# Performance work log

Hardware: AMD Instinct MI355X
Metric: run time of the kernel (lower is better)

Reference implementation:

```python
import jax, jax.numpy as jnp
import numpy as np


def setup_inputs() -> dict:
    key0 = jax.random.key(0)
    kq, kk, kv = jax.random.split(key0, 3)
    B, H, L, S, D = 2, 8, 2048, 2048, 64
    query = jax.random.normal(kq, (B, H, L, D), dtype=jnp.float32)
    key = jax.random.normal(kk, (B, H, S, D), dtype=jnp.float32)
    value = jax.random.normal(kv, (B, H, S, D), dtype=jnp.float32)
    return {"query": query, "key": key, "value": value}


def reference(query, key, value):
    # Original computes matmul(q[b,h,l,1,d,1], k[b,h,1,s,1,d]) -> [B,H,L,S,D,D]
    # outer products, divides by sqrt(query.shape[-1]) AFTER unsqueeze (==1, no-op),
    # then sums dims (4,5). That is algebraically exactly rowsum(q)*rowsum(k).
    qsum = query.sum(axis=-1)                       # [B,H,L]
    ksum = key.sum(axis=-1)                         # [B,H,S]
    score = qsum[..., :, None] * ksum[..., None, :]  # [B,H,L,S]
    attn = jax.nn.softmax(score, axis=-1)            # softmax over S
    out = jnp.einsum('bhls,bhsd->bhld', attn, value)  # [B,H,L,D]
    return out
```

## Files before the change

kernel.cpp:

```cpp
#include <hip/hip_runtime.h>
#include <hip/hip_bf16.h>

#define BH 16
#define L 2048
#define S 2048
#define DD 64
#define BM 64
#define BK 64
#define LDSPAD 8
#define LDW (BK + LDSPAD)

typedef __attribute__((ext_vector_type(4))) float f32x4;
typedef __bf16 bf16x8 __attribute__((ext_vector_type(8)));

union FragU {
  bf16x8 f;
  __hip_bfloat162 h2[4];
};

__device__ inline __hip_bfloat162 exp2pack(float al2, float nsl2, float k0,
                                           float k1, float& d) {
  float e0 = __builtin_amdgcn_exp2f(fmaf(al2, k0, nsl2));
  float e1 = __builtin_amdgcn_exp2f(fmaf(al2, k1, nsl2));
  d += e0 + e1;
  return __float22bfloat162_rn(make_float2(e0, e1));
}

__global__ __launch_bounds__(256) void prep_kernel(
    const float* __restrict__ k, const float* __restrict__ v,
    float* __restrict__ ks, __hip_bfloat16* __restrict__ vt) {
  __shared__ __hip_bfloat16 tile[DD][LDW];
  int t = threadIdx.x;
  if (blockIdx.x < 2048) {
    int g = blockIdx.x * 256 + t;
    int row = g >> 4;
    int l16 = g & 15;
    float4 x = reinterpret_cast<const float4*>(k + (size_t)row * DD)[l16];
    float s = x.x + x.y + x.z + x.w;
    s += __shfl_xor(s, 1);
    s += __shfl_xor(s, 2);
    s += __shfl_xor(s, 4);
    s += __shfl_xor(s, 8);
    if (l16 == 0) ks[row] = s;
  } else {
    int bid = blockIdx.x - 2048;
    int s0 = (bid & 31) * 64;
    int bh = bid >> 5;
    int srow = t >> 4;
    int d4 = (t & 15) * 4;
#pragma unroll
    for (int kk = 0; kk < 4; ++kk) {
      int s = srow + kk * 16;
      float4 val = *reinterpret_cast<const float4*>(
          v + ((size_t)(bh * S + s0 + s)) * DD + d4);
      tile[d4 + 0][s] = __float2bfloat16(val.x);
      tile[d4 + 1][s] = __float2bfloat16(val.y);
      tile[d4 + 2][s] = __float2bfloat16(val.z);
      tile[d4 + 3][s] = __float2bfloat16(val.w);
    }
    __syncthreads();
    int dd = t >> 3;
    int j = t & 7;
#pragma unroll
    for (int kk = 0; kk < 2; ++kk) {
      int d = dd + kk * 32;
      uint4 val = *reinterpret_cast<const uint4*>(&tile[d][j * 8]);
      *reinterpret_cast<uint4*>(vt + ((size_t)(bh * DD + d)) * S + s0 + j * 8) =
          val;
    }
  }
}

__global__ __launch_bounds__(256) void attn_kernel(
    const float* __restrict__ q, const __hip_bfloat16* __restrict__ vt,
    const float* __restrict__ ks, float* __restrict__ out) {
  int l0 = blockIdx.x * BM;
  int bh = blockIdx.y;

  __shared__ __hip_bfloat16 ldsVT[2][DD][LDW];
  __shared__ float a_row[BM];
  __shared__ float red[16];

  int t = threadIdx.x;
  int lane = t & 63;
  int w = t >> 6;
  int m = lane & 15;
  int qd = lane >> 4;

  const __hip_bfloat16* vtb = vt + (size_t)bh * DD * S;
  const float* ksb = ks + (size_t)bh * S;

  int vd = t >> 3;
  int vj = t & 7;

  uint4 v0 = *reinterpret_cast<const uint4*>(vtb + (size_t)vd * S + vj * 8);
  uint4 v1 =
      *reinterpret_cast<const uint4*>(vtb + (size_t)(vd + 32) * S + vj * 8);
  float4 kA0 = *reinterpret_cast<const float4*>(ksb + qd * 8);
  float4 kA1 = *reinterpret_cast<const float4*>(ksb + qd * 8 + 4);
  float4 kB0 = *reinterpret_cast<const float4*>(ksb + 32 + qd * 8);
  float4 kB1 = *reinterpret_cast<const float4*>(ksb + 32 + qd * 8 + 4);

  {
    int r = t >> 2;
    int p = t & 3;
    const float* qp = q + ((size_t)(bh * L + l0 + r)) * DD + p * 16;
    float4 x0 = reinterpret_cast<const float4*>(qp)[0];
    float4 x1 = reinterpret_cast<const float4*>(qp)[1];
    float4 x2 = reinterpret_cast<const float4*>(qp)[2];
    float4 x3 = reinterpret_cast<const float4*>(qp)[3];
    float s = (x0.x + x0.y + x0.z + x0.w) + (x1.x + x1.y + x1.z + x1.w) +
              (x2.x + x2.y + x2.z + x2.w) + (x3.x + x3.y + x3.z + x3.w);
    s += __shfl_xor(s, 1);
    s += __shfl_xor(s, 2);
    if (p == 0) a_row[r] = s;
  }

  {
    const float* kp = ksb + t * 8;
    float4 y0 = reinterpret_cast<const float4*>(kp)[0];
    float4 y1 = reinterpret_cast<const float4*>(kp)[1];
    float mx = fmaxf(fmaxf(fmaxf(y0.x, y0.y), fmaxf(y0.z, y0.w)),
                     fmaxf(fmaxf(y1.x, y1.y), fmaxf(y1.z, y1.w)));
    float mn = fminf(fminf(fminf(y0.x, y0.y), fminf(y0.z, y0.w)),
                     fminf(fminf(y1.x, y1.y), fminf(y1.z, y1.w)));
#pragma unroll
    for (int off = 1; off < 64; off <<= 1) {
      mx = fmaxf(mx, __shfl_xor(mx, off));
      mn = fminf(mn, __shfl_xor(mn, off));
    }
    if (lane == 0) {
      red[w] = mx;
      red[8 + w] = mn;
    }
  }
  __syncthreads();

  float kmax = fmaxf(fmaxf(red[0], red[1]), fmaxf(red[2], red[3]));
  float kmin = fminf(fminf(red[8], red[9]), fminf(red[10], red[11]));
  float ar = a_row[w * 16 + m];
  float sel = (ar > 0.f) ? kmax : kmin;
  const float LOG2E = 1.44269504088896f;
  float al2 = ar * LOG2E;
  float nsl2 = -al2 * sel;

  float dsum = 0.f;
  f32x4 acc[4];
#pragma unroll
  for (int c = 0; c < 4; ++c) acc[c] = (f32x4){0.f, 0.f, 0.f, 0.f};

  for (int it = 0; it < 32; ++it) {
    int bufi = it & 1;
    *reinterpret_cast<uint4*>(&ldsVT[bufi][vd][vj * 8]) = v0;
    *reinterpret_cast<uint4*>(&ldsVT[bufi][vd + 32][vj * 8]) = v1;
    __syncthreads();

    int s0n = (it < 31) ? (it + 1) * BK : 31 * BK;
    v0 = *reinterpret_cast<const uint4*>(vtb + (size_t)vd * S + s0n + vj * 8);
    v1 = *reinterpret_cast<const uint4*>(vtb + (size_t)(vd + 32) * S + s0n +
                                         vj * 8);

    FragU f0, f1;
    f0.h2[0] = exp2pack(al2, nsl2, kA0.x, kA0.y, dsum);
    f0.h2[1] = exp2pack(al2, nsl2, kA0.z, kA0.w, dsum);
    f0.h2[2] = exp2pack(al2, nsl2, kA1.x, kA1.y, dsum);
    f0.h2[3] = exp2pack(al2, nsl2, kA1.z, kA1.w, dsum);
    f1.h2[0] = exp2pack(al2, nsl2, kB0.x, kB0.y, dsum);
    f1.h2[1] = exp2pack(al2, nsl2, kB0.z, kB0.w, dsum);
    f1.h2[2] = exp2pack(al2, nsl2, kB1.x, kB1.y, dsum);
    f1.h2[3] = exp2pack(al2, nsl2, kB1.z, kB1.w, dsum);

    kA0 = *reinterpret_cast<const float4*>(ksb + s0n + qd * 8);
    kA1 = *reinterpret_cast<const float4*>(ksb + s0n + qd * 8 + 4);
    kB0 = *reinterpret_cast<const float4*>(ksb + s0n + 32 + qd * 8);
    kB1 = *reinterpret_cast<const float4*>(ksb + s0n + 32 + qd * 8 + 4);

#pragma unroll
    for (int c = 0; c < 4; ++c) {
      uint4 bu0 =
          *reinterpret_cast<const uint4*>(&ldsVT[bufi][c * 16 + m][qd * 8]);
      acc[c] = __builtin_amdgcn_mfma_f32_16x16x32_bf16(
          f0.f, __builtin_bit_cast(bf16x8, bu0), acc[c], 0, 0, 0);
      uint4 bu1 = *reinterpret_cast<const uint4*>(
          &ldsVT[bufi][c * 16 + m][32 + qd * 8]);
      acc[c] = __builtin_amdgcn_mfma_f32_16x16x32_bf16(
          f1.f, __builtin_bit_cast(bf16x8, bu1), acc[c], 0, 0, 0);
    }
  }

  float dt = dsum;
  dt += __shfl_xor(dt, 16);
  dt += __shfl_xor(dt, 32);
  float inv[4];
#pragma unroll
  for (int i = 0; i < 4; ++i) inv[i] = 1.0f / __shfl(dt, qd * 4 + i);

  float* ob = out + ((size_t)(bh * L + l0 + w * 16)) * DD;
#pragma unroll
  for (int c = 0; c < 4; ++c) {
#pragma unroll
    for (int i = 0; i < 4; ++i) {
      ob[(size_t)(qd * 4 + i) * DD + c * 16 + m] = acc[c][i] * inv[i];
    }
  }
}

extern "C" void kernel_launch(void* const* d_in, const int* in_sizes, int n_in,
                              void* d_out, int out_size, void* d_ws,
                              size_t ws_size, hipStream_t stream) {
  const float* q = (const float*)d_in[0];
  const float* k = (const float*)d_in[1];
  const float* v = (const float*)d_in[2];
  float* out = (float*)d_out;
  float* ws = (float*)d_ws;

  float* ks = ws;
  __hip_bfloat16* vt = (__hip_bfloat16*)(ws + BH * S);

  prep_kernel<<<2048 + 512, 256, 0, stream>>>(k, v, ks, vt);
  attn_kernel<<<dim3(L / BM, BH), 256, 0, stream>>>(q, vt, ks, out);
}
```

Baseline: 96.84 us.

## Split S across waves with 32-row blocks and LDS cross-wave reduction

Restructures the attention kernel so each block handles 32 query rows and each of the four waves processes a quarter of the S dimension. V^T fragments are read directly from global memory into registers instead of being staged through double-buffered LDS with per-iteration barriers. Partial numerators and denominators are combined through LDS at the end, and the output is written with vectorized stores. This doubles the grid and removes the loop barriers, in exchange for more global/L2 traffic for V per block and a final LDS reduction.

```diff
diff --git a/kernel.cpp b/kernel.cpp
--- a/kernel.cpp
+++ b/kernel.cpp
@@ -5,10 +5,10 @@
 #define L 2048
 #define S 2048
 #define DD 64
-#define BM 64
-#define BK 64
+#define BMB 32
+#define NPITCH 68
 #define LDSPAD 8
-#define LDW (BK + LDSPAD)
+#define LDW (DD + LDSPAD)
 
 typedef __attribute__((ext_vector_type(4))) float f32x4;
 typedef __bf16 bf16x8 __attribute__((ext_vector_type(8)));
@@ -71,14 +71,15 @@
   }
 }
 
-__global__ __launch_bounds__(256) void attn_kernel(
+__global__ __launch_bounds__(256, 4) void attn_kernel(
     const float* __restrict__ q, const __hip_bfloat16* __restrict__ vt,
     const float* __restrict__ ks, float* __restrict__ out) {
-  int l0 = blockIdx.x * BM;
+  int l0 = blockIdx.x * BMB;
   int bh = blockIdx.y;
 
-  __shared__ __hip_bfloat16 ldsVT[2][DD][LDW];
-  __shared__ float a_row[BM];
+  __shared__ float numLDS[4][BMB][NPITCH];
+  __shared__ float dLDS[4][BMB];
+  __shared__ float a_row[BMB];
   __shared__ float red[16];
 
   int t = threadIdx.x;
@@ -87,35 +88,21 @@
   int m = lane & 15;
   int qd = lane >> 4;
 
+  const float* ksb = ks + (size_t)bh * S;
   const __hip_bfloat16* vtb = vt + (size_t)bh * DD * S;
-  const float* ksb = ks + (size_t)bh * S;
-
-  int vd = t >> 3;
-  int vj = t & 7;
-
-  uint4 v0 = *reinterpret_cast<const uint4*>(vtb + (size_t)vd * S + vj * 8);
-  uint4 v1 =
-      *reinterpret_cast<const uint4*>(vtb + (size_t)(vd + 32) * S + vj * 8);
-  float4 kA0 = *reinterpret_cast<const float4*>(ksb + qd * 8);
-  float4 kA1 = *reinterpret_cast<const float4*>(ksb + qd * 8 + 4);
-  float4 kB0 = *reinterpret_cast<const float4*>(ksb + 32 + qd * 8);
-  float4 kB1 = *reinterpret_cast<const float4*>(ksb + 32 + qd * 8 + 4);
 
   {
-    int r = t >> 2;
-    int p = t & 3;
-    const float* qp = q + ((size_t)(bh * L + l0 + r)) * DD + p * 16;
+    int r = t >> 3;
+    int p = t & 7;
+    const float* qp = q + ((size_t)(bh * L + l0 + r)) * DD + p * 8;
     float4 x0 = reinterpret_cast<const float4*>(qp)[0];
     float4 x1 = reinterpret_cast<const float4*>(qp)[1];
-    float4 x2 = reinterpret_cast<const float4*>(qp)[2];
-    float4 x3 = reinterpret_cast<const float4*>(qp)[3];
-    float s = (x0.x + x0.y + x0.z + x0.w) + (x1.x + x1.y + x1.z + x1.w) +
-              (x2.x + x2.y + x2.z + x2.w) + (x3.x + x3.y + x3.z + x3.w);
+    float s = (x0.x + x0.y + x0.z + x0.w) + (x1.x + x1.y + x1.z + x1.w);
     s += __shfl_xor(s, 1);
     s += __shfl_xor(s, 2);
+    s += __shfl_xor(s, 4);
     if (p == 0) a_row[r] = s;
   }
-
   {
     const float* kp = ksb + t * 8;
     float4 y0 = reinterpret_cast<const float4*>(kp)[0];
@@ -138,70 +125,130 @@
 
   float kmax = fmaxf(fmaxf(red[0], red[1]), fmaxf(red[2], red[3]));
   float kmin = fminf(fminf(red[8], red[9]), fminf(red[10], red[11]));
-  float ar = a_row[w * 16 + m];
-  float sel = (ar > 0.f) ? kmax : kmin;
   const float LOG2E = 1.44269504088896f;
-  float al2 = ar * LOG2E;
-  float nsl2 = -al2 * sel;
-
-  float dsum = 0.f;
-  f32x4 acc[4];
-#pragma unroll
-  for (int c = 0; c < 4; ++c) acc[c] = (f32x4){0.f, 0.f, 0.f, 0.f};
-
-  for (int it = 0; it < 32; ++it) {
-    int bufi = it & 1;
-    *reinterpret_cast<uint4*>(&ldsVT[bufi][vd][vj * 8]) = v0;
-    *reinterpret_cast<uint4*>(&ldsVT[bufi][vd + 32][vj * 8]) = v1;
-    __syncthreads();
-
-    int s0n = (it < 31) ? (it + 1) * BK : 31 * BK;
-    v0 = *reinterpret_cast<const uint4*>(vtb + (size_t)vd * S + s0n + vj * 8);
-    v1 = *reinterpret_cast<const uint4*>(vtb + (size_t)(vd + 32) * S + s0n +
-                                         vj * 8);
-
-    FragU f0, f1;
-    f0.h2[0] = exp2pack(al2, nsl2, kA0.x, kA0.y, dsum);
-    f0.h2[1] = exp2pack(al2, nsl2, kA0.z, kA0.w, dsum);
-    f0.h2[2] = exp2pack(al2, nsl2, kA1.x, kA1.y, dsum);
-    f0.h2[3] = exp2pack(al2, nsl2, kA1.z, kA1.w, dsum);
-    f1.h2[0] = exp2pack(al2, nsl2, kB0.x, kB0.y, dsum);
-    f1.h2[1] = exp2pack(al2, nsl2, kB0.z, kB0.w, dsum);
-    f1.h2[2] = exp2pack(al2, nsl2, kB1.x, kB1.y, dsum);
-    f1.h2[3] = exp2pack(al2, nsl2, kB1.z, kB1.w, dsum);
-
-    kA0 = *reinterpret_cast<const float4*>(ksb + s0n + qd * 8);
-    kA1 = *reinterpret_cast<const float4*>(ksb + s0n + qd * 8 + 4);
-    kB0 = *reinterpret_cast<const float4*>(ksb + s0n + 32 + qd * 8);
-    kB1 = *reinterpret_cast<const float4*>(ksb + s0n + 32 + qd * 8 + 4);
-
-#pragma unroll
-    for (int c = 0; c < 4; ++c) {
-      uint4 bu0 =
-          *reinterpret_cast<const uint4*>(&ldsVT[bufi][c * 16 + m][qd * 8]);
-      acc[c] = __builtin_amdgcn_mfma_f32_16x16x32_bf16(
-          f0.f, __builtin_bit_cast(bf16x8, bu0), acc[c], 0, 0, 0);
-      uint4 bu1 = *reinterpret_cast<const uint4*>(
-          &ldsVT[bufi][c * 16 + m][32 + qd * 8]);
-      acc[c] = __builtin_amdgcn_mfma_f32_16x16x32_bf16(
-          f1.f, __builtin_bit_cast(bf16x8, bu1), acc[c], 0, 0, 0);
-    }
-  }
-
-  float dt = dsum;
-  dt += __shfl_xor(dt, 16);
-  dt += __shfl_xor(dt, 32);
-  float inv[4];
-#pragma unroll
-  for (int i = 0; i < 4; ++i) inv[i] = 1.0f / __shfl(dt, qd * 4 + i);
-
-  float* ob = out + ((size_t)(bh * L + l0 + w * 16)) * DD;
-#pragma unroll
-  for (int c = 0; c < 4; ++c) {
-#pragma unroll
-    for (int i = 0; i < 4; ++i) {
-      ob[(size_t)(qd * 4 + i) * DD + c * 16 + m] = acc[c][i] * inv[i];
-    }
+  float ar0 = a_row[m];
+  float ar1 = a_row[16 + m];
+  float al20 = ar0 * LOG2E, al21 = ar1 * LOG2E;
+  float nsl20 = -al20 * ((ar0 > 0.f) ? kmax : kmin);
+  float nsl21 = -al21 * ((ar1 > 0.f) ? kmax : kmin);
+
+  f32x4 acc[2][4];
+#pragma unroll
+  for (int a = 0; a < 2; ++a)
+#pragma unroll
+    for (int c = 0; c < 4; ++c) acc[a][c] = (f32x4){0.f, 0.f, 0.f, 0.f};
+  float ds0a = 0.f, ds0b = 0.f, ds1a = 0.f, ds1b = 0.f;
+
+  const __hip_bfloat16* bp0 = vtb + (size_t)(0 * 16 + m) * S + qd * 8;
+  const __hip_bfloat16* bp1 = vtb + (size_t)(1 * 16 + m) * S + qd * 8;
+  const __hip_bfloat16* bp2 = vtb + (size_t)(2 * 16 + m) * S + qd * 8;
+  const __hip_bfloat16* bp3 = vtb + (size_t)(3 * 16 + m) * S + qd * 8;
+
+  int sw = w * (S / 4);
+  for (int it = 0; it < (S / 4) / 64; ++it) {
+    int sb = sw + it * 64;
+    float4 kA0 = *reinterpret_cast<const float4*>(ksb + sb + qd * 8);
+    float4 kA1 = *reinterpret_cast<const float4*>(ksb + sb + qd * 8 + 4);
+    float4 kB0 = *reinterpret_cast<const float4*>(ksb + sb + 32 + qd * 8);
+    float4 kB1 = *reinterpret_cast<const float4*>(ksb + sb + 32 + qd * 8 + 4);
+    uint4 b00 = *reinterpret_cast<const uint4*>(bp0 + sb);
+    uint4 b01 = *reinterpret_cast<const uint4*>(bp1 + sb);
+    uint4 b02 = *reinterpret_cast<const uint4*>(bp2 + sb);
+    uint4 b03 = *reinterpret_cast<const uint4*>(bp3 + sb);
+    uint4 b10 = *reinterpret_cast<const uint4*>(bp0 + sb + 32);
+    uint4 b11 = *reinterpret_cast<const uint4*>(bp1 + sb + 32);
+    uint4 b12 = *reinterpret_cast<const uint4*>(bp2 + sb + 32);
+    uint4 b13 = *reinterpret_cast<const uint4*>(bp3 + sb + 32);
+
+    FragU e00, e01, e10, e11;
+    e00.h2[0] = exp2pack(al20, nsl20, kA0.x, kA0.y, ds0a);
+    e00.h2[1] = exp2pack(al20, nsl20, kA0.z, kA0.w, ds0a);
+    e00.h2[2] = exp2pack(al20, nsl20, kA1.x, kA1.y, ds0a);
+    e00.h2[3] = exp2pack(al20, nsl20, kA1.z, kA1.w, ds0a);
+    e01.h2[0] = exp2pack(al20, nsl20, kB0.x, kB0.y, ds0b);
+    e01.h2[1] = exp2pack(al20, nsl20, kB0.z, kB0.w, ds0b);
+    e01.h2[2] = exp2pack(al20, nsl20, kB1.x, kB1.y, ds0b);
+    e01.h2[3] = exp2pack(al20, nsl20, kB1.z, kB1.w, ds0b);
+    e10.h2[0] = exp2pack(al21, nsl21, kA0.x, kA0.y, ds1a);
+    e10.h2[1] = exp2pack(al21, nsl21, kA0.z, kA0.w, ds1a);
+    e10.h2[2] = exp2pack(al21, nsl21, kA1.x, kA1.y, ds1a);
+    e10.h2[3] = exp2pack(al21, nsl21, kA1.z, kA1.w, ds1a);
+    e11.h2[0] = exp2pack(al21, nsl21, kB0.x, kB0.y, ds1b);
+    e11.h2[1] = exp2pack(al21, nsl21, kB0.z, kB0.w, ds1b);
+    e11.h2[2] = exp2pack(al21, nsl21, kB1.x, kB1.y, ds1b);
+    e11.h2[3] = exp2pack(al21, nsl21, kB1.z, kB1.w, ds1b);
+
+    acc[0][0] = __builtin_amdgcn_mfma_f32_16x16x32_bf16(
+        e00.f, __builtin_bit_cast(bf16x8, b00), acc[0][0], 0, 0, 0);
+    acc[0][1] = __builtin_amdgcn_mfma_f32_16x16x32_bf16(
+        e00.f, __builtin_bit_cast(bf16x8, b01), acc[0][1], 0, 0, 0);
+    acc[0][2] = __builtin_amdgcn_mfma_f32_16x16x32_bf16(
+        e00.f, __builtin_bit_cast(bf16x8, b02), acc[0][2], 0, 0, 0);
+    acc[0][3] = __builtin_amdgcn_mfma_f32_16x16x32_bf16(
+        e00.f, __builtin_bit_cast(bf16x8, b03), acc[0][3], 0, 0, 0);
+    acc[1][0] = __builtin_amdgcn_mfma_f32_16x16x32_bf16(
+        e10.f, __builtin_bit_cast(bf16x8, b00), acc[1][0], 0, 0, 0);
+    acc[1][1] = __builtin_amdgcn_mfma_f32_16x16x32_bf16(
+        e10.f, __builtin_bit_cast(bf16x8, b01), acc[1][1], 0, 0, 0);
+    acc[1][2] = __builtin_amdgcn_mfma_f32_16x16x32_bf16(
+        e10.f, __builtin_bit_cast(bf16x8, b02), acc[1][2], 0, 0, 0);
+    acc[1][3] = __builtin_amdgcn_mfma_f32_16x16x32_bf16(
+        e10.f, __builtin_bit_cast(bf16x8, b03), acc[1][3], 0, 0, 0);
+    acc[0][0] = __builtin_amdgcn_mfma_f32_16x16x32_bf16(
+        e01.f, __builtin_bit_cast(bf16x8, b10), acc[0][0], 0, 0, 0);
+    acc[0][1] = __builtin_amdgcn_mfma_f32_16x16x32_bf16(
+        e01.f, __builtin_bit_cast(bf16x8, b11), acc[0][1], 0, 0, 0);
+    acc[0][2] = __builtin_amdgcn_mfma_f32_16x16x32_bf16(
+        e01.f, __builtin_bit_cast(bf16x8, b12), acc[0][2], 0, 0, 0);
+    acc[0][3] = __builtin_amdgcn_mfma_f32_16x16x32_bf16(
+        e01.f, __builtin_bit_cast(bf16x8, b13), acc[0][3], 0, 0, 0);
+    acc[1][0] = __builtin_amdgcn_mfma_f32_16x16x32_bf16(
+        e11.f, __builtin_bit_cast(bf16x8, b10), acc[1][0], 0, 0, 0);
+    acc[1][1] = __builtin_amdgcn_mfma_f32_16x16x32_bf16(
+        e11.f, __builtin_bit_cast(bf16x8, b11), acc[1][1], 0, 0, 0);
+    acc[1][2] = __builtin_amdgcn_mfma_f32_16x16x32_bf16(
+        e11.f, __builtin_bit_cast(bf16x8, b12), acc[1][2], 0, 0, 0);
+    acc[1][3] = __builtin_amdgcn_mfma_f32_16x16x32_bf16(
+        e11.f, __builtin_bit_cast(bf16x8, b13), acc[1][3], 0, 0, 0);
+  }
+
+  float ds0 = ds0a + ds0b;
+  float ds1 = ds1a + ds1b;
+  ds0 += __shfl_xor(ds0, 16);
+  ds0 += __shfl_xor(ds0, 32);
+  ds1 += __shfl_xor(ds1, 16);
+  ds1 += __shfl_xor(ds1, 32);
+  if (qd == 0) {
+    dLDS[w][m] = ds0;
+    dLDS[w][16 + m] = ds1;
+  }
+#pragma unroll
+  for (int a = 0; a < 2; ++a)
+#pragma unroll
+    for (int c = 0; c < 4; ++c)
+#pragma unroll
+      for (int i = 0; i < 4; ++i)
+        numLDS[w][a * 16 + qd * 4 + i][c * 16 + m] = acc[a][c][i];
+  __syncthreads();
+
+  {
+    int r = t >> 3;
+    int cg = (t & 7) * 8;
+    float4 n0 = *reinterpret_cast<const float4*>(&numLDS[0][r][cg]);
+    float4 n1 = *reinterpret_cast<const float4*>(&numLDS[0][r][cg + 4]);
+#pragma unroll
+    for (int ww = 1; ww < 4; ++ww) {
+      float4 p0 = *reinterpret_cast<const float4*>(&numLDS[ww][r][cg]);
+      float4 p1 = *reinterpret_cast<const float4*>(&numLDS[ww][r][cg + 4]);
+      n0.x += p0.x; n0.y += p0.y; n0.z += p0.z; n0.w += p0.w;
+      n1.x += p1.x; n1.y += p1.y; n1.z += p1.z; n1.w += p1.w;
+    }
+    float inv = 1.0f / (dLDS[0][r] + dLDS[1][r] + dLDS[2][r] + dLDS[3][r]);
+    n0.x *= inv; n0.y *= inv; n0.z *= inv; n0.w *= inv;
+    n1.x *= inv; n1.y *= inv; n1.z *= inv; n1.w *= inv;
+    float* ob = out + ((size_t)(bh * L + l0 + r)) * DD + cg;
+    reinterpret_cast<float4*>(ob)[0] = n0;
+    reinterpret_cast<float4*>(ob)[1] = n1;
   }
 }
 
@@ -218,5 +265,5 @@
   __hip_bfloat16* vt = (__hip_bfloat16*)(ws + BH * S);
 
   prep_kernel<<<2048 + 512, 256, 0, stream>>>(k, v, ks, vt);
-  attn_kernel<<<dim3(L / BM, BH), 256, 0, stream>>>(q, vt, ks, out);
-}
+  attn_kernel<<<dim3(L / BMB, BH), 256, 0, stream>>>(q, vt, ks, out);
+}
```

After: 110.9 us. 14.5% more time.

## Store transposed V in contiguous 64x64 tiles and swizzle block-to-head mapping

Applied to the files above, without the earlier changes.

The prep kernel now writes the bf16 transposed V as contiguous 8KB tiles per (head, 64-key chunk) rather than strided rows of length S. Each attention block therefore fetches a fully contiguous 8KB chunk per iteration. The grid is flattened and remapped so that consecutive blocks cover different heads, interleaved to spread them across XCDs for better L2 locality. The extra bit-twiddling is minor, but the cross-XCD cache effects are hard to predict.

```diff
diff --git a/kernel.cpp b/kernel.cpp
--- a/kernel.cpp
+++ b/kernel.cpp
@@ -44,8 +44,9 @@
     if (l16 == 0) ks[row] = s;
   } else {
     int bid = blockIdx.x - 2048;
-    int s0 = (bid & 31) * 64;
-    int bh = bid >> 5;
+    int bh = (bid & 7) * 2 + ((bid >> 3) & 1);
+    int st = bid >> 4;
+    int s0 = st * 64;
     int srow = t >> 4;
     int d4 = (t & 15) * 4;
 #pragma unroll
@@ -59,14 +60,14 @@
       tile[d4 + 3][s] = __float2bfloat16(val.w);
     }
     __syncthreads();
+    __hip_bfloat16* tb = vt + ((size_t)(bh * 32 + st)) * (DD * 64);
     int dd = t >> 3;
     int j = t & 7;
 #pragma unroll
     for (int kk = 0; kk < 2; ++kk) {
       int d = dd + kk * 32;
       uint4 val = *reinterpret_cast<const uint4*>(&tile[d][j * 8]);
-      *reinterpret_cast<uint4*>(vt + ((size_t)(bh * DD + d)) * S + s0 + j * 8) =
-          val;
+      *reinterpret_cast<uint4*>(tb + d * 64 + j * 8) = val;
     }
   }
 }
@@ -74,8 +75,9 @@
 __global__ __launch_bounds__(256) void attn_kernel(
     const float* __restrict__ q, const __hip_bfloat16* __restrict__ vt,
     const float* __restrict__ ks, float* __restrict__ out) {
-  int l0 = blockIdx.x * BM;
-  int bh = blockIdx.y;
+  int bx = blockIdx.x;
+  int bh = (bx & 7) * 2 + ((bx >> 3) & 1);
+  int l0 = (bx >> 4) * BM;
 
   __shared__ __hip_bfloat16 ldsVT[2][DD][LDW];
   __shared__ float a_row[BM];
@@ -87,15 +89,11 @@
   int m = lane & 15;
   int qd = lane >> 4;
 
-  const __hip_bfloat16* vtb = vt + (size_t)bh * DD * S;
+  const __hip_bfloat16* vtb = vt + ((size_t)bh * 32) * (DD * 64);
   const float* ksb = ks + (size_t)bh * S;
 
-  int vd = t >> 3;
-  int vj = t & 7;
-
-  uint4 v0 = *reinterpret_cast<const uint4*>(vtb + (size_t)vd * S + vj * 8);
-  uint4 v1 =
-      *reinterpret_cast<const uint4*>(vtb + (size_t)(vd + 32) * S + vj * 8);
+  uint4 v0 = *reinterpret_cast<const uint4*>(vtb + t * 8);
+  uint4 v1 = *reinterpret_cast<const uint4*>(vtb + 2048 + t * 8);
   float4 kA0 = *reinterpret_cast<const float4*>(ksb + qd * 8);
   float4 kA1 = *reinterpret_cast<const float4*>(ksb + qd * 8 + 4);
   float4 kB0 = *reinterpret_cast<const float4*>(ksb + 32 + qd * 8);
@@ -151,14 +149,15 @@
 
   for (int it = 0; it < 32; ++it) {
     int bufi = it & 1;
-    *reinterpret_cast<uint4*>(&ldsVT[bufi][vd][vj * 8]) = v0;
-    *reinterpret_cast<uint4*>(&ldsVT[bufi][vd + 32][vj * 8]) = v1;
+    *reinterpret_cast<uint4*>(&ldsVT[bufi][t >> 3][(t & 7) * 8]) = v0;
+    *reinterpret_cast<uint4*>(&ldsVT[bufi][32 + (t >> 3)][(t & 7) * 8]) = v1;
     __syncthreads();
 
-    int s0n = (it < 31) ? (it + 1) * BK : 31 * BK;
-    v0 = *reinterpret_cast<const uint4*>(vtb + (size_t)vd * S + s0n + vj * 8);
-    v1 = *reinterpret_cast<const uint4*>(vtb + (size_t)(vd + 32) * S + s0n +
-                                         vj * 8);
+    int itn = (it < 31) ? it + 1 : 31;
+    const __hip_bfloat16* tn = vtb + (size_t)itn * (DD * 64);
+    v0 = *reinterpret_cast<const uint4*>(tn + t * 8);
+    v1 = *reinterpret_cast<const uint4*>(tn + 2048 + t * 8);
+    int s0n = itn * BK;
 
     FragU f0, f1;
     f0.h2[0] = exp2pack(al2, nsl2, kA0.x, kA0.y, dsum);
@@ -218,5 +217,5 @@
   __hip_bfloat16* vt = (__hip_bfloat16*)(ws + BH * S);
 
   prep_kernel<<<2048 + 512, 256, 0, stream>>>(k, v, ks, vt);
-  attn_kernel<<<dim3(L / BM, BH), 256, 0, stream>>>(q, vt, ks, out);
-}
+  attn_kernel<<<(L / BM) * BH, 256, 0, stream>>>(q, vt, ks, out);
+}
```

Measured after the change: 100.3 us. 1.04x slower.
